# Kernel tuning notes

Hardware: AMD Instinct MI355X
Metric: run time of the kernel (lower is better)

Reference implementation:

```python
import jax, jax.numpy as jnp
import numpy as np
import math

N_EMBD = 1024
N_HEAD = 16
B, T = 2, 2048


def new_gelu(x):
    # GPT-2 tanh-approx GELU (matches torch module exactly)
    return 0.5 * x * (1.0 + jnp.tanh(jnp.sqrt(2.0 / jnp.pi) * (x + 0.044715 * x ** 3)))


def layer_norm(x, w, b, eps=1e-5):
    mu = jnp.mean(x, axis=-1, keepdims=True)
    var = jnp.var(x, axis=-1, keepdims=True)
    return (x - mu) * jax.lax.rsqrt(var + eps) * w + b


def setup_inputs() -> dict:
    key = jax.random.key(0)
    ks = jax.random.split(key, 8)
    C = N_EMBD
    s = 0.02
    return {
        "x": jax.random.normal(ks[0], (B, T, C), dtype=jnp.float32),
        "ln1_w": jnp.ones((C,), jnp.float32),
        "ln1_b": jnp.zeros((C,), jnp.float32),
        "attn_w": s * jax.random.normal(ks[1], (C, 3 * C), jnp.float32),
        "attn_b": jnp.zeros((3 * C,), jnp.float32),
        "attn_proj_w": s * jax.random.normal(ks[2], (C, C), jnp.float32),
        "attn_proj_b": jnp.zeros((C,), jnp.float32),
        "ln2_w": jnp.ones((C,), jnp.float32),
        "ln2_b": jnp.zeros((C,), jnp.float32),
        "fc_w": s * jax.random.normal(ks[3], (C, 4 * C), jnp.float32),
        "fc_b": jnp.zeros((4 * C,), jnp.float32),
        "mlp_proj_w": s * jax.random.normal(ks[4], (4 * C, C), jnp.float32),
        "mlp_proj_b": jnp.zeros((C,), jnp.float32),
    }


def block_forward(x, ln1_w, ln1_b, attn_w, attn_b, attn_proj_w, attn_proj_b,
                  ln2_w, ln2_b, fc_w, fc_b, mlp_proj_w, mlp_proj_b):
    Bm, Tm, C = x.shape
    H = N_HEAD
    D = C // H
    # --- self attention (pre-LN) ---
    h = layer_norm(x, ln1_w, ln1_b)
    qkv = h @ attn_w + attn_b  # [B,T,3C]
    q, k, v = jnp.split(qkv, 3, axis=-1)
    q = q.reshape(Bm, Tm, H, D).transpose(0, 2, 1, 3)  # [B,H,T,D]
    k = k.reshape(Bm, Tm, H, D).transpose(0, 2, 1, 3)
    v = v.reshape(Bm, Tm, H, D).transpose(0, 2, 1, 3)
    att = jnp.einsum('bhqd,bhkd->bhqk', q, k) * (1.0 / math.sqrt(D))
    att = jax.nn.softmax(att, axis=-1)  # NOTE: no causal mask in source
    y = jnp.einsum('bhqk,bhkd->bhqd', att, v)
    y = y.transpose(0, 2, 1, 3).reshape(Bm, Tm, C)
    x = x + (y @ attn_proj_w + attn_proj_b)
    # --- MLP ---
    h = layer_norm(x, ln2_w, ln2_b)
    h = new_gelu(h @ fc_w + fc_b)
    x = x + (h @ mlp_proj_w + mlp_proj_b)
    return x


def reference(x, ln1_w, ln1_b, attn_w, attn_b, attn_proj_w, attn_proj_b,
              ln2_w, ln2_b, fc_w, fc_b, mlp_proj_w, mlp_proj_b):
    return block_forward(x, ln1_w, ln1_b, attn_w, attn_b, attn_proj_w, attn_proj_b,
                         ln2_w, ln2_b, fc_w, fc_b, mlp_proj_w, mlp_proj_b)
```

## Files before the change

### kernel.cpp

```cpp
#include <hip/hip_runtime.h>

typedef __attribute__((ext_vector_type(4)))  float  f32x4;
typedef __attribute__((ext_vector_type(16))) float  f32x16;
typedef __attribute__((ext_vector_type(8)))  short  s16x8;
typedef __attribute__((ext_vector_type(4)))  short  s16x4;
typedef __attribute__((ext_vector_type(4)))  unsigned u32x4;
typedef __attribute__((ext_vector_type(2)))  unsigned u32x2;
typedef __attribute__((ext_vector_type(2)))  int    i32x2;

__device__ __forceinline__ short f2bf(float f) {
    unsigned u = __builtin_bit_cast(unsigned, f);
    u += 0x7fff + ((u >> 16) & 1);
    return (short)(u >> 16);
}

__device__ __forceinline__ void load_lds16(const void* g, void* l) {
    __builtin_amdgcn_global_load_lds(
        (const __attribute__((address_space(1))) unsigned int*)g,
        (__attribute__((address_space(3))) unsigned int*)l, 16, 0, 0);
}

__device__ __forceinline__ float tsum32(const f32x16& a, const f32x16& b) {
    float u[16];
#pragma unroll
    for (int i = 0; i < 16; i++) u[i] = a[i] + b[i];
#pragma unroll
    for (int i = 0; i < 8; i++) u[i] += u[i + 8];
#pragma unroll
    for (int i = 0; i < 4; i++) u[i] += u[i + 4];
    return (u[0] + u[2]) + (u[1] + u[3]);
}

__global__ __launch_bounds__(256) void transpose_cast(const float* __restrict__ W,
                                                      short* __restrict__ Wt,
                                                      int K, int N) {
    __shared__ float t[32][33];
    int n0 = blockIdx.x * 32, k0 = blockIdx.y * 32;
    int tx = threadIdx.x & 31, ty = threadIdx.x >> 5;
#pragma unroll
    for (int i = 0; i < 4; i++)
        t[ty + 8 * i][tx] = W[(size_t)(k0 + ty + 8 * i) * N + n0 + tx];
    __syncthreads();
#pragma unroll
    for (int i = 0; i < 4; i++)
        Wt[(size_t)(n0 + ty + 8 * i) * K + k0 + tx] = f2bf(t[tx][ty + 8 * i]);
}

__global__ __launch_bounds__(256) void ln_kernel(const float* __restrict__ x,
                                                 const float* __restrict__ w,
                                                 const float* __restrict__ b,
                                                 short* __restrict__ out) {
    int row = blockIdx.x;
    int tid = threadIdx.x;
    const float4 v = ((const float4*)(x + (size_t)row * 1024))[tid];
    float s  = v.x + v.y + v.z + v.w;
    float ss = v.x * v.x + v.y * v.y + v.z * v.z + v.w * v.w;
#pragma unroll
    for (int o = 32; o > 0; o >>= 1) {
        s  += __shfl_down(s, o);
        ss += __shfl_down(ss, o);
    }
    __shared__ float rs[4], rq[4];
    int wave = tid >> 6, lane = tid & 63;
    if (lane == 0) { rs[wave] = s; rq[wave] = ss; }
    __syncthreads();
    float tot = rs[0] + rs[1] + rs[2] + rs[3];
    float tq  = rq[0] + rq[1] + rq[2] + rq[3];
    float mu   = tot * (1.f / 1024.f);
    float var  = tq * (1.f / 1024.f) - mu * mu;
    float rstd = rsqrtf(var + 1e-5f);
    const float4 wv = ((const float4*)w)[tid];
    const float4 bv = ((const float4*)b)[tid];
    s16x4 o;
    o[0] = f2bf((v.x - mu) * rstd * wv.x + bv.x);
    o[1] = f2bf((v.y - mu) * rstd * wv.y + bv.y);
    o[2] = f2bf((v.z - mu) * rstd * wv.z + bv.z);
    o[3] = f2bf((v.w - mu) * rstd * wv.w + bv.w);
    ((s16x4*)(out + (size_t)row * 1024))[tid] = o;
}

__device__ __forceinline__ void xcd_remap(int& bx, int& by) {
    int gx = gridDim.x, gy = gridDim.y;
    int hwid = blockIdx.y * gx + blockIdx.x;
    int xcd = hwid & 7, rank = hwid >> 3;
    int pan = gx >> 3;
    bx = xcd * pan + rank / gy;
    by = rank % gy;
}

template <typename OUT_T, bool GELU, bool RES, bool SCALE_Q, bool VSPLIT>
__global__ __launch_bounds__(256) void gemm_bt(const short* __restrict__ A,
                                               const short* __restrict__ Bt,
                                               const float* __restrict__ bias,
                                               const float* __restrict__ res,
                                               OUT_T* __restrict__ C,
                                               short* __restrict__ vtg,
                                               int M, int N, int K) {
    __shared__ __align__(16) short As[2][128 * 32];
    __shared__ __align__(16) short Bs[2][128 * 32];
    int tid = threadIdx.x;
    int bx, by;
    xcd_remap(bx, by);
    int m0 = by * 128, n0 = bx * 128;
    int wave = tid >> 6, lane = tid & 63;
    int wr = wave >> 1, wc = wave & 1;
    int g = lane >> 4, q = lane & 15;
    f32x4 acc[4][4] = {};
    const short* Ab = A + (size_t)m0 * K;
    const short* Bb = Bt + (size_t)n0 * K;
    int srow = tid >> 2;
    int scol = (tid & 3) * 8;
    auto stage = [&](int bi, int k0) {
        load_lds16(Ab + (size_t)srow * K + k0 + scol, &As[bi][tid * 8]);
        load_lds16(Ab + (size_t)(srow + 64) * K + k0 + scol, &As[bi][2048 + tid * 8]);
        load_lds16(Bb + (size_t)srow * K + k0 + scol, &Bs[bi][tid * 8]);
        load_lds16(Bb + (size_t)(srow + 64) * K + k0 + scol, &Bs[bi][2048 + tid * 8]);
    };
    int nk = K >> 5;
    stage(0, 0);
    __syncthreads();
    for (int kk = 0; kk < nk; ++kk) {
        int cur = kk & 1;
        if (kk + 1 < nk) stage(cur ^ 1, (kk + 1) << 5);
        s16x8 a[4], bf[4];
#pragma unroll
        for (int mi = 0; mi < 4; mi++)
            a[mi] = *(const s16x8*)(&As[cur][(wr * 64 + mi * 16 + q) * 32 + g * 8]);
#pragma unroll
        for (int ni = 0; ni < 4; ni++)
            bf[ni] = *(const s16x8*)(&Bs[cur][(wc * 64 + ni * 16 + q) * 32 + g * 8]);
#pragma unroll
        for (int mi = 0; mi < 4; mi++)
#pragma unroll
            for (int ni = 0; ni < 4; ni++)
                acc[mi][ni] = __builtin_amdgcn_mfma_f32_16x16x32_bf16(a[mi], bf[ni], acc[mi][ni], 0, 0, 0);
        __syncthreads();
    }
#pragma unroll
    for (int mi = 0; mi < 4; mi++) {
#pragma unroll
        for (int ni = 0; ni < 4; ni++) {
            int row = m0 + wr * 64 + mi * 16 + g * 4;
            int col = n0 + wc * 64 + ni * 16 + q;
            float bb = bias[col];
            if (VSPLIT && col >= 2048) {
                int d = col & 63;
                int bh2 = ((row >> 11) << 4) + ((col - 2048) >> 6);
                s16x4 o;
#pragma unroll
                for (int r = 0; r < 4; r++) o[r] = f2bf(acc[mi][ni][r] + bb);
                *(s16x4*)&vtg[((size_t)bh2 * 64 + d) * 2048 + (row & 2047)] = o;
            } else {
#pragma unroll
                for (int r = 0; r < 4; r++) {
                    float v = acc[mi][ni][r] + bb;
                    if (RES) v += res[(size_t)(row + r) * N + col];
                    if (GELU) {
                        float aa = 0.7978845608028654f * (v + 0.044715f * v * v * v);
                        float th = 1.f - 2.f / (__expf(2.f * aa) + 1.f);
                        v = 0.5f * v * (1.f + th);
                    }
                    if (SCALE_Q && col < 1024) v *= 0.18033688011112042f;
                    if constexpr (sizeof(OUT_T) == 2)
                        C[(size_t)(row + r) * N + col] = f2bf(v);
                    else
                        C[(size_t)(row + r) * N + col] = v;
                }
            }
        }
    }
}

__global__ __launch_bounds__(256) void gemm_bt_sk(const short* __restrict__ A,
                                                  const short* __restrict__ Bt,
                                                  float* __restrict__ part,
                                                  int M, int N, int K, int Klen) {
    __shared__ __align__(16) short As[2][128 * 32];
    __shared__ __align__(16) short Bs[2][128 * 32];
    int tid = threadIdx.x;
    int bx, by;
    xcd_remap(bx, by);
    int m0 = by * 128, n0 = bx * 128;
    int kz = blockIdx.z;
    int wave = tid >> 6, lane = tid & 63;
    int wr = wave >> 1, wc = wave & 1;
    int g = lane >> 4, q = lane & 15;
    f32x4 acc[4][4] = {};
    const short* Ab = A + (size_t)m0 * K;
    const short* Bb = Bt + (size_t)n0 * K;
    int srow = tid >> 2;
    int scol = (tid & 3) * 8;
    auto stage = [&](int bi, int k0) {
        load_lds16(Ab + (size_t)srow * K + k0 + scol, &As[bi][tid * 8]);
        load_lds16(Ab + (size_t)(srow + 64) * K + k0 + scol, &As[bi][2048 + tid * 8]);
        load_lds16(Bb + (size_t)srow * K + k0 + scol, &Bs[bi][tid * 8]);
        load_lds16(Bb + (size_t)(srow + 64) * K + k0 + scol, &Bs[bi][2048 + tid * 8]);
    };
    int kbase = kz * Klen;
    int nk = Klen >> 5;
    stage(0, kbase);
    __syncthreads();
    for (int kk = 0; kk < nk; ++kk) {
        int cur = kk & 1;
        if (kk + 1 < nk) stage(cur ^ 1, kbase + ((kk + 1) << 5));
        s16x8 a[4], bf[4];
#pragma unroll
        for (int mi = 0; mi < 4; mi++)
            a[mi] = *(const s16x8*)(&As[cur][(wr * 64 + mi * 16 + q) * 32 + g * 8]);
#pragma unroll
        for (int ni = 0; ni < 4; ni++)
            bf[ni] = *(const s16x8*)(&Bs[cur][(wc * 64 + ni * 16 + q) * 32 + g * 8]);
#pragma unroll
        for (int mi = 0; mi < 4; mi++)
#pragma unroll
            for (int ni = 0; ni < 4; ni++)
                acc[mi][ni] = __builtin_amdgcn_mfma_f32_16x16x32_bf16(a[mi], bf[ni], acc[mi][ni], 0, 0, 0);
        __syncthreads();
    }
    float* pb = part + (size_t)kz * M * N;
#pragma unroll
    for (int mi = 0; mi < 4; mi++) {
#pragma unroll
        for (int ni = 0; ni < 4; ni++) {
            int row = m0 + wr * 64 + mi * 16 + g * 4;
            int col = n0 + wc * 64 + ni * 16 + q;
#pragma unroll
            for (int r = 0; r < 4; r++)
                pb[(size_t)(row + r) * N + col] = acc[mi][ni][r];
        }
    }
}

template <int SK>
__global__ __launch_bounds__(256) void reduce_sk(const float* __restrict__ part,
                                                 const float* __restrict__ bias,
                                                 const float* __restrict__ res,
                                                 float* __restrict__ out,
                                                 int MN, int N) {
    int tot = MN >> 2;
    int nb4 = (N >> 2) - 1;
    for (int i = blockIdx.x * 256 + threadIdx.x; i < tot; i += gridDim.x * 256) {
        float4 s = ((const float4*)part)[i];
#pragma unroll
        for (int k = 1; k < SK; k++) {
            float4 p = ((const float4*)(part + (size_t)k * MN))[i];
            s.x += p.x; s.y += p.y; s.z += p.z; s.w += p.w;
        }
        float4 bv = ((const float4*)bias)[i & nb4];
        float4 rv = ((const float4*)res)[i];
        float4 o;
        o.x = s.x + bv.x + rv.x;
        o.y = s.y + bv.y + rv.y;
        o.z = s.z + bv.z + rv.z;
        o.w = s.w + bv.w + rv.w;
        ((float4*)out)[i] = o;
    }
}

__global__ __launch_bounds__(128) void attn_kernel(const short* __restrict__ qkv,
                                                   const short* __restrict__ Vtg,
                                                   short* __restrict__ y) {
    const int T = 2048, C3 = 3072;
    int wg = blockIdx.x;
    int mapped = (wg & 7) * 128 + (wg >> 3);
    int bh = mapped >> 5, qt = mapped & 31;
    int b = bh >> 4, h = bh & 15;
    int tid = threadIdx.x, lane = tid & 63, wave = tid >> 6;
    int ql = lane & 31, hi = lane >> 5;
    const short* base = qkv + (size_t)b * T * C3;

    int qrow = qt * 64 + wave * 32 + ql;
    const short* qp = base + (size_t)qrow * C3 + h * 64;
    s16x8 qf[4];
#pragma unroll
    for (int s = 0; s < 4; s++)
        qf[s] = *(const s16x8*)(qp + ((2 * s + hi) << 3));

    __shared__ __align__(16) short Ks[2][64 * 64];
    __shared__ __align__(16) short Vs[2][64 * 64];

    int srow = tid >> 3, sc8 = tid & 7;
    const short* kp = base + 1024 + h * 64 + (size_t)srow * C3 + ((sc8 ^ (srow & 7)) << 3);
    const short* vp = Vtg + ((size_t)bh * 64 + srow) * T + ((sc8 ^ (srow & 7)) << 3);

    auto stage = [&](int bi) {
#pragma unroll
        for (int i = 0; i < 4; i++) {
            load_lds16(kp + (size_t)(16 * i) * C3, &Ks[bi][i * 1024 + tid * 8]);
            load_lds16(vp + (size_t)(16 * i) * T,  &Vs[bi][i * 1024 + tid * 8]);
        }
    };

    float lst = 0.f;
    f32x16 accY0 = {}, accY1 = {};
    int swz = ql & 7;

    stage(0);
    for (int t = 0; t < 32; ++t) {
        int cur = t & 1;
        __syncthreads();
        if (t < 31) {
            kp += 64 * C3;
            vp += 64;
            stage(cur ^ 1);
        }
        f32x16 s0 = {}, s1 = {};
        const short* kb0 = &Ks[cur][ql * 64];
        const short* kb1 = &Ks[cur][(32 + ql) * 64];
        __builtin_amdgcn_s_setprio(1);
#pragma unroll
        for (int s = 0; s < 4; s++) {
            int c = ((2 * s + hi) ^ swz) << 3;
            s16x8 k0 = *(const s16x8*)(kb0 + c);
            s16x8 k1 = *(const s16x8*)(kb1 + c);
            s0 = __builtin_amdgcn_mfma_f32_32x32x16_bf16(k0, qf[s], s0, 0, 0, 0);
            s1 = __builtin_amdgcn_mfma_f32_32x32x16_bf16(k1, qf[s], s1, 0, 0, 0);
        }
        __builtin_amdgcn_s_setprio(0);
#pragma unroll
        for (int r = 0; r < 16; r++) s0[r] = exp2f(s0[r]);
#pragma unroll
        for (int r = 0; r < 16; r++) s1[r] = exp2f(s1[r]);
        float ps = tsum32(s0, s1);
        ps += __shfl_xor(ps, 32);
        lst += ps;
        s16x8 pb[4];
#pragma unroll
        for (int s = 0; s < 4; s++) {
            int tt = (s & 1) * 8;
            unsigned lo0, lo1, hi0, hi1;
            if (s < 2) {
                asm("v_cvt_pk_bf16_f32 %0, %1, %2" : "=v"(lo0) : "v"(s0[tt + 0]), "v"(s0[tt + 1]));
                asm("v_cvt_pk_bf16_f32 %0, %1, %2" : "=v"(lo1) : "v"(s0[tt + 2]), "v"(s0[tt + 3]));
                asm("v_cvt_pk_bf16_f32 %0, %1, %2" : "=v"(hi0) : "v"(s0[tt + 4]), "v"(s0[tt + 5]));
                asm("v_cvt_pk_bf16_f32 %0, %1, %2" : "=v"(hi1) : "v"(s0[tt + 6]), "v"(s0[tt + 7]));
            } else {
                asm("v_cvt_pk_bf16_f32 %0, %1, %2" : "=v"(lo0) : "v"(s1[tt + 0]), "v"(s1[tt + 1]));
                asm("v_cvt_pk_bf16_f32 %0, %1, %2" : "=v"(lo1) : "v"(s1[tt + 2]), "v"(s1[tt + 3]));
                asm("v_cvt_pk_bf16_f32 %0, %1, %2" : "=v"(hi0) : "v"(s1[tt + 4]), "v"(s1[tt + 5]));
                asm("v_cvt_pk_bf16_f32 %0, %1, %2" : "=v"(hi1) : "v"(s1[tt + 6]), "v"(s1[tt + 7]));
            }
            i32x2 r0 = __builtin_amdgcn_permlane32_swap((int)hi0, (int)lo0, false, false);
            i32x2 r1 = __builtin_amdgcn_permlane32_swap((int)hi1, (int)lo1, false, false);
            u32x4 w;
            w[0] = (unsigned)r0[1]; w[1] = (unsigned)r1[1];
            w[2] = (unsigned)r0[0]; w[3] = (unsigned)r1[0];
            pb[s] = __builtin_bit_cast(s16x8, w);
        }
        const short* vb0 = &Vs[cur][ql * 64];
        const short* vb1 = &Vs[cur][(32 + ql) * 64];
        __builtin_amdgcn_s_setprio(1);
#pragma unroll
        for (int s = 0; s < 4; s++) {
            int c = ((2 * s + hi) ^ swz) << 3;
            s16x8 v0 = *(const s16x8*)(vb0 + c);
            s16x8 v1 = *(const s16x8*)(vb1 + c);
            accY0 = __builtin_amdgcn_mfma_f32_32x32x16_bf16(v0, pb[s], accY0, 0, 0, 0);
            accY1 = __builtin_amdgcn_mfma_f32_32x32x16_bf16(v1, pb[s], accY1, 0, 0, 0);
        }
        __builtin_amdgcn_s_setprio(0);
    }
    float linv = 1.f / lst;
    short* yrow = y + ((size_t)b * T + qrow) * 1024 + h * 64;
#pragma unroll
    for (int r = 0; r < 4; r++) {
        unsigned w0, w1, w2, w3;
        float a0 = accY0[4 * r] * linv, a1 = accY0[4 * r + 1] * linv;
        float a2 = accY0[4 * r + 2] * linv, a3 = accY0[4 * r + 3] * linv;
        float b0 = accY1[4 * r] * linv, b1 = accY1[4 * r + 1] * linv;
        float b2 = accY1[4 * r + 2] * linv, b3 = accY1[4 * r + 3] * linv;
        asm("v_cvt_pk_bf16_f32 %0, %1, %2" : "=v"(w0) : "v"(a0), "v"(a1));
        asm("v_cvt_pk_bf16_f32 %0, %1, %2" : "=v"(w1) : "v"(a2), "v"(a3));
        asm("v_cvt_pk_bf16_f32 %0, %1, %2" : "=v"(w2) : "v"(b0), "v"(b1));
        asm("v_cvt_pk_bf16_f32 %0, %1, %2" : "=v"(w3) : "v"(b2), "v"(b3));
        u32x2 p0; p0[0] = w0; p0[1] = w1;
        u32x2 p1; p1[0] = w2; p1[1] = w3;
        *(u32x2*)(yrow + 8 * r + 4 * hi)      = p0;
        *(u32x2*)(yrow + 32 + 8 * r + 4 * hi) = p1;
    }
}

extern "C" void kernel_launch(void* const* d_in, const int* in_sizes, int n_in,
                              void* d_out, int out_size, void* d_ws, size_t ws_size,
                              hipStream_t stream) {
    const float* x           = (const float*)d_in[0];
    const float* ln1_w       = (const float*)d_in[1];
    const float* ln1_b       = (const float*)d_in[2];
    const float* attn_w      = (const float*)d_in[3];
    const float* attn_b      = (const float*)d_in[4];
    const float* attn_proj_w = (const float*)d_in[5];
    const float* attn_proj_b = (const float*)d_in[6];
    const float* ln2_w       = (const float*)d_in[7];
    const float* ln2_b       = (const float*)d_in[8];
    const float* fc_w        = (const float*)d_in[9];
    const float* fc_b        = (const float*)d_in[10];
    const float* mlp_proj_w  = (const float*)d_in[11];
    const float* mlp_proj_b  = (const float*)d_in[12];

    const int M = 4096;

    size_t off = 0;
    char* wsb = (char*)d_ws;
    auto alloc = [&](size_t bytes) {
        void* p = wsb + off;
        off += (bytes + 255) & ~(size_t)255;
        return p;
    };
    short* wt_attn  = (short*)alloc(3072ull * 1024 * 2);
    short* wt_proj  = (short*)alloc(1024ull * 1024 * 2);
    short* wt_fc    = (short*)alloc(4096ull * 1024 * 2);
    short* wt_mproj = (short*)alloc(1024ull * 4096 * 2);
    short* h1       = (short*)alloc((size_t)M * 1024 * 2);
    short* qkvb     = (short*)alloc((size_t)M * 3072 * 2);
    short* yb       = (short*)alloc((size_t)M * 1024 * 2);
    float* x1       = (float*)alloc((size_t)M * 1024 * 4);
    short* vtg      = (short*)alloc((size_t)M * 1024 * 2);
    short* h2       = qkvb;

    size_t base_off = off;
    int SK = 0;
    if (ws_size >= base_off + 4ull * M * 1024 * 4) SK = 4;
    else if (ws_size >= base_off + 2ull * M * 1024 * 4) SK = 2;
    float* part = (float*)(wsb + base_off);

    transpose_cast<<<dim3(3072 / 32, 1024 / 32), 256, 0, stream>>>(attn_w, wt_attn, 1024, 3072);
    transpose_cast<<<dim3(1024 / 32, 1024 / 32), 256, 0, stream>>>(attn_proj_w, wt_proj, 1024, 1024);
    transpose_cast<<<dim3(4096 / 32, 1024 / 32), 256, 0, stream>>>(fc_w, wt_fc, 1024, 4096);
    transpose_cast<<<dim3(1024 / 32, 4096 / 32), 256, 0, stream>>>(mlp_proj_w, wt_mproj, 4096, 1024);

    ln_kernel<<<M, 256, 0, stream>>>(x, ln1_w, ln1_b, h1);
    gemm_bt<short, false, false, true, true><<<dim3(3072 / 128, M / 128), 256, 0, stream>>>(
        h1, wt_attn, attn_b, nullptr, qkvb, vtg, M, 3072, 1024);
    attn_kernel<<<1024, 128, 0, stream>>>(qkvb, vtg, yb);
    gemm_bt<float, false, true, false, false><<<dim3(1024 / 128, M / 128), 256, 0, stream>>>(
        yb, wt_proj, attn_proj_b, x, x1, nullptr, M, 1024, 1024);
    ln_kernel<<<M, 256, 0, stream>>>(x1, ln2_w, ln2_b, h1);
    gemm_bt<short, true, false, false, false><<<dim3(4096 / 128, M / 128), 256, 0, stream>>>(
        h1, wt_fc, fc_b, nullptr, h2, nullptr, M, 4096, 1024);

    if (SK == 4) {
        gemm_bt_sk<<<dim3(1024 / 128, M / 128, 4), 256, 0, stream>>>(
            h2, wt_mproj, part, M, 1024, 4096, 1024);
        reduce_sk<4><<<2048, 256, 0, stream>>>(part, mlp_proj_b, x1, (float*)d_out, M * 1024, 1024);
    } else if (SK == 2) {
        gemm_bt_sk<<<dim3(1024 / 128, M / 128, 2), 256, 0, stream>>>(
            h2, wt_mproj, part, M, 1024, 4096, 2048);
        reduce_sk<2><<<2048, 256, 0, stream>>>(part, mlp_proj_b, x1, (float*)d_out, M * 1024, 1024);
    } else {
        gemm_bt<float, false, true, false, false><<<dim3(1024 / 128, M / 128), 256, 0, stream>>>(
            h2, wt_mproj, mlp_proj_b, x1, (float*)d_out, nullptr, M, 1024, 4096);
    }
}
```

Baseline: 292.3 us.

## Enlarge attention tiles to 128 queries and 128 keys; fuse weight transposes

The attention kernel moves from 64-query/64-key tiles with 2 waves to 128-query/128-key tiles with 4 waves. Each K/V tile staged in LDS is now shared by more query rows, and there are half as many loop iterations and barriers. The four weight transpose launches are merged into one kernel that picks its matrix by block index, saving launch overhead. The cost is more LDS and registers per block, which lowers occupancy, and only 512 blocks in the attention grid.

```diff
diff --git a/kernel.cpp b/kernel.cpp
--- a/kernel.cpp
+++ b/kernel.cpp
@@ -31,11 +31,23 @@
     return (u[0] + u[2]) + (u[1] + u[3]);
 }
 
-__global__ __launch_bounds__(256) void transpose_cast(const float* __restrict__ W,
-                                                      short* __restrict__ Wt,
-                                                      int K, int N) {
+__global__ __launch_bounds__(256) void transpose_all(const float* __restrict__ w0,
+                                                     const float* __restrict__ w1,
+                                                     const float* __restrict__ w2,
+                                                     const float* __restrict__ w3,
+                                                     short* __restrict__ t0s,
+                                                     short* __restrict__ t1s,
+                                                     short* __restrict__ t2s,
+                                                     short* __restrict__ t3s) {
     __shared__ float t[32][33];
-    int n0 = blockIdx.x * 32, k0 = blockIdx.y * 32;
+    int id = blockIdx.x;
+    const float* W; short* Wt; int K, N;
+    if (id < 3072)      { W = w0; Wt = t0s; K = 1024; N = 3072; }
+    else if (id < 4096) { W = w1; Wt = t1s; K = 1024; N = 1024; id -= 3072; }
+    else if (id < 8192) { W = w2; Wt = t2s; K = 1024; N = 4096; id -= 4096; }
+    else                { W = w3; Wt = t3s; K = 4096; N = 1024; id -= 8192; }
+    int ntn = N >> 5;
+    int n0 = (id % ntn) * 32, k0 = (id / ntn) * 32;
     int tx = threadIdx.x & 31, ty = threadIdx.x >> 5;
 #pragma unroll
     for (int i = 0; i < 4; i++)
@@ -257,37 +269,38 @@
     }
 }
 
-__global__ __launch_bounds__(128) void attn_kernel(const short* __restrict__ qkv,
+__global__ __launch_bounds__(256) void attn_kernel(const short* __restrict__ qkv,
                                                    const short* __restrict__ Vtg,
                                                    short* __restrict__ y) {
     const int T = 2048, C3 = 3072;
     int wg = blockIdx.x;
-    int mapped = (wg & 7) * 128 + (wg >> 3);
-    int bh = mapped >> 5, qt = mapped & 31;
+    int mapped = (wg & 7) * 64 + (wg >> 3);
+    int bh = mapped >> 4, qt = mapped & 15;
     int b = bh >> 4, h = bh & 15;
     int tid = threadIdx.x, lane = tid & 63, wave = tid >> 6;
     int ql = lane & 31, hi = lane >> 5;
     const short* base = qkv + (size_t)b * T * C3;
 
-    int qrow = qt * 64 + wave * 32 + ql;
+    int qrow = qt * 128 + wave * 32 + ql;
     const short* qp = base + (size_t)qrow * C3 + h * 64;
     s16x8 qf[4];
 #pragma unroll
     for (int s = 0; s < 4; s++)
         qf[s] = *(const s16x8*)(qp + ((2 * s + hi) << 3));
 
-    __shared__ __align__(16) short Ks[2][64 * 64];
-    __shared__ __align__(16) short Vs[2][64 * 64];
-
-    int srow = tid >> 3, sc8 = tid & 7;
-    const short* kp = base + 1024 + h * 64 + (size_t)srow * C3 + ((sc8 ^ (srow & 7)) << 3);
-    const short* vp = Vtg + ((size_t)bh * 64 + srow) * T + ((sc8 ^ (srow & 7)) << 3);
+    __shared__ __align__(16) short Ks[2][128 * 64];
+    __shared__ __align__(16) short Vs[2][64 * 128];
+
+    const short* kp = base + 1024 + h * 64 + (size_t)(tid >> 3) * C3
+                    + (((tid & 7) ^ ((tid >> 3) & 7)) << 3);
+    const short* vp = Vtg + ((size_t)bh * 64 + (tid >> 4)) * T
+                    + (((tid & 15) ^ ((tid >> 4) & 7)) << 3);
 
     auto stage = [&](int bi) {
 #pragma unroll
         for (int i = 0; i < 4; i++) {
-            load_lds16(kp + (size_t)(16 * i) * C3, &Ks[bi][i * 1024 + tid * 8]);
-            load_lds16(vp + (size_t)(16 * i) * T,  &Vs[bi][i * 1024 + tid * 8]);
+            load_lds16(kp + (size_t)(32 * i) * C3, &Ks[bi][i * 2048 + tid * 8]);
+            load_lds16(vp + (size_t)(16 * i) * T,  &Vs[bi][i * 2048 + tid * 8]);
         }
     };
 
@@ -296,50 +309,50 @@
     int swz = ql & 7;
 
     stage(0);
-    for (int t = 0; t < 32; ++t) {
+    for (int t = 0; t < 16; ++t) {
         int cur = t & 1;
         __syncthreads();
-        if (t < 31) {
-            kp += 64 * C3;
-            vp += 64;
+        if (t < 15) {
+            kp += 128 * C3;
+            vp += 128;
             stage(cur ^ 1);
         }
-        f32x16 s0 = {}, s1 = {};
-        const short* kb0 = &Ks[cur][ql * 64];
-        const short* kb1 = &Ks[cur][(32 + ql) * 64];
+        f32x16 sc0 = {}, sc1 = {}, sc2 = {}, sc3 = {};
         __builtin_amdgcn_s_setprio(1);
 #pragma unroll
         for (int s = 0; s < 4; s++) {
             int c = ((2 * s + hi) ^ swz) << 3;
-            s16x8 k0 = *(const s16x8*)(kb0 + c);
-            s16x8 k1 = *(const s16x8*)(kb1 + c);
-            s0 = __builtin_amdgcn_mfma_f32_32x32x16_bf16(k0, qf[s], s0, 0, 0, 0);
-            s1 = __builtin_amdgcn_mfma_f32_32x32x16_bf16(k1, qf[s], s1, 0, 0, 0);
+            s16x8 k0 = *(const s16x8*)(&Ks[cur][(ql)       * 64] + c);
+            s16x8 k1 = *(const s16x8*)(&Ks[cur][(32 + ql)  * 64] + c);
+            s16x8 k2 = *(const s16x8*)(&Ks[cur][(64 + ql)  * 64] + c);
+            s16x8 k3 = *(const s16x8*)(&Ks[cur][(96 + ql)  * 64] + c);
+            sc0 = __builtin_amdgcn_mfma_f32_32x32x16_bf16(k0, qf[s], sc0, 0, 0, 0);
+            sc1 = __builtin_amdgcn_mfma_f32_32x32x16_bf16(k1, qf[s], sc1, 0, 0, 0);
+            sc2 = __builtin_amdgcn_mfma_f32_32x32x16_bf16(k2, qf[s], sc2, 0, 0, 0);
+            sc3 = __builtin_amdgcn_mfma_f32_32x32x16_bf16(k3, qf[s], sc3, 0, 0, 0);
         }
         __builtin_amdgcn_s_setprio(0);
 #pragma unroll
-        for (int r = 0; r < 16; r++) s0[r] = exp2f(s0[r]);
-#pragma unroll
-        for (int r = 0; r < 16; r++) s1[r] = exp2f(s1[r]);
-        float ps = tsum32(s0, s1);
+        for (int r = 0; r < 16; r++) sc0[r] = exp2f(sc0[r]);
+#pragma unroll
+        for (int r = 0; r < 16; r++) sc1[r] = exp2f(sc1[r]);
+#pragma unroll
+        for (int r = 0; r < 16; r++) sc2[r] = exp2f(sc2[r]);
+#pragma unroll
+        for (int r = 0; r < 16; r++) sc3[r] = exp2f(sc3[r]);
+        float ps = tsum32(sc0, sc1) + tsum32(sc2, sc3);
         ps += __shfl_xor(ps, 32);
         lst += ps;
-        s16x8 pb[4];
-#pragma unroll
-        for (int s = 0; s < 4; s++) {
+        s16x8 pb[8];
+#pragma unroll
+        for (int s = 0; s < 8; s++) {
+            const f32x16& sg = (s < 2) ? sc0 : (s < 4) ? sc1 : (s < 6) ? sc2 : sc3;
             int tt = (s & 1) * 8;
             unsigned lo0, lo1, hi0, hi1;
-            if (s < 2) {
-                asm("v_cvt_pk_bf16_f32 %0, %1, %2" : "=v"(lo0) : "v"(s0[tt + 0]), "v"(s0[tt + 1]));
-                asm("v_cvt_pk_bf16_f32 %0, %1, %2" : "=v"(lo1) : "v"(s0[tt + 2]), "v"(s0[tt + 3]));
-                asm("v_cvt_pk_bf16_f32 %0, %1, %2" : "=v"(hi0) : "v"(s0[tt + 4]), "v"(s0[tt + 5]));
-                asm("v_cvt_pk_bf16_f32 %0, %1, %2" : "=v"(hi1) : "v"(s0[tt + 6]), "v"(s0[tt + 7]));
-            } else {
-                asm("v_cvt_pk_bf16_f32 %0, %1, %2" : "=v"(lo0) : "v"(s1[tt + 0]), "v"(s1[tt + 1]));
-                asm("v_cvt_pk_bf16_f32 %0, %1, %2" : "=v"(lo1) : "v"(s1[tt + 2]), "v"(s1[tt + 3]));
-                asm("v_cvt_pk_bf16_f32 %0, %1, %2" : "=v"(hi0) : "v"(s1[tt + 4]), "v"(s1[tt + 5]));
-                asm("v_cvt_pk_bf16_f32 %0, %1, %2" : "=v"(hi1) : "v"(s1[tt + 6]), "v"(s1[tt + 7]));
-            }
+            asm("v_cvt_pk_bf16_f32 %0, %1, %2" : "=v"(lo0) : "v"(sg[tt + 0]), "v"(sg[tt + 1]));
+            asm("v_cvt_pk_bf16_f32 %0, %1, %2" : "=v"(lo1) : "v"(sg[tt + 2]), "v"(sg[tt + 3]));
+            asm("v_cvt_pk_bf16_f32 %0, %1, %2" : "=v"(hi0) : "v"(sg[tt + 4]), "v"(sg[tt + 5]));
+            asm("v_cvt_pk_bf16_f32 %0, %1, %2" : "=v"(hi1) : "v"(sg[tt + 6]), "v"(sg[tt + 7]));
             i32x2 r0 = __builtin_amdgcn_permlane32_swap((int)hi0, (int)lo0, false, false);
             i32x2 r1 = __builtin_amdgcn_permlane32_swap((int)hi1, (int)lo1, false, false);
             u32x4 w;
@@ -347,11 +360,11 @@
             w[2] = (unsigned)r0[0]; w[3] = (unsigned)r1[0];
             pb[s] = __builtin_bit_cast(s16x8, w);
         }
-        const short* vb0 = &Vs[cur][ql * 64];
-        const short* vb1 = &Vs[cur][(32 + ql) * 64];
+        const short* vb0 = &Vs[cur][ql * 128];
+        const short* vb1 = &Vs[cur][(32 + ql) * 128];
         __builtin_amdgcn_s_setprio(1);
 #pragma unroll
-        for (int s = 0; s < 4; s++) {
+        for (int s = 0; s < 8; s++) {
             int c = ((2 * s + hi) ^ swz) << 3;
             s16x8 v0 = *(const s16x8*)(vb0 + c);
             s16x8 v1 = *(const s16x8*)(vb1 + c);
@@ -423,15 +436,13 @@
     else if (ws_size >= base_off + 2ull * M * 1024 * 4) SK = 2;
     float* part = (float*)(wsb + base_off);
 
-    transpose_cast<<<dim3(3072 / 32, 1024 / 32), 256, 0, stream>>>(attn_w, wt_attn, 1024, 3072);
-    transpose_cast<<<dim3(1024 / 32, 1024 / 32), 256, 0, stream>>>(attn_proj_w, wt_proj, 1024, 1024);
-    transpose_cast<<<dim3(4096 / 32, 1024 / 32), 256, 0, stream>>>(fc_w, wt_fc, 1024, 4096);
-    transpose_cast<<<dim3(1024 / 32, 4096 / 32), 256, 0, stream>>>(mlp_proj_w, wt_mproj, 4096, 1024);
+    transpose_all<<<12288, 256, 0, stream>>>(attn_w, attn_proj_w, fc_w, mlp_proj_w,
+                                             wt_attn, wt_proj, wt_fc, wt_mproj);
 
     ln_kernel<<<M, 256, 0, stream>>>(x, ln1_w, ln1_b, h1);
     gemm_bt<short, false, false, true, true><<<dim3(3072 / 128, M / 128), 256, 0, stream>>>(
         h1, wt_attn, attn_b, nullptr, qkvb, vtg, M, 3072, 1024);
-    attn_kernel<<<1024, 128, 0, stream>>>(qkvb, vtg, yb);
+    attn_kernel<<<512, 256, 0, stream>>>(qkvb, vtg, yb);
     gemm_bt<float, false, true, false, false><<<dim3(1024 / 128, M / 128), 256, 0, stream>>>(
         yb, wt_proj, attn_proj_b, x, x1, nullptr, M, 1024, 1024);
     ln_kernel<<<M, 256, 0, stream>>>(x1, ln2_w, ln2_b, h1);
```

Result: slower. 307.2 us (+5.1%).
